# Performance work log

Measured on AMD Instinct MI355X. Metric: run time of the kernel, lower is better.

Reference implementation:

```python
import jax, jax.numpy as jnp
import numpy as np

EPS = float(np.finfo(np.float32).eps)
B, MZ, NF = 8192, 2000, 2048
W_INT, W_PROB, W_WS, W_MORGAN = 0.1, 0.3, 0.5, 0.1
POS_W = 5.0


def _bce_logits(x, y):
    # numerically-stable BCEWithLogits, elementwise
    return jnp.maximum(x, 0.0) - x * y + jnp.log1p(jnp.exp(-jnp.abs(x)))


def setup_inputs() -> dict:
    key = jax.random.key(0)
    k = jax.random.split(key, 6)
    return {
        "pred_intensities": jax.random.normal(k[0], (B, MZ), jnp.float32),
        "pred_probs_logits": jax.random.normal(k[1], (B, MZ), jnp.float32),
        "pred_morgan_logits": jax.random.normal(k[2], (B, NF), jnp.float32),
        "true_intensities": jax.random.uniform(k[3], (B, MZ), dtype=jnp.float32),
        "true_probs": jax.random.uniform(k[4], (B, MZ), dtype=jnp.float32),
        "true_morgan": jax.random.randint(k[5], (B, NF), 0, 2).astype(jnp.int32),
    }


def reference(pred_intensities, pred_probs_logits, pred_morgan_logits,
              true_intensities, true_probs, true_morgan):
    # --- prob loss: BCEWithLogits with positive-class upweighting ---
    bce = _bce_logits(pred_probs_logits, true_probs)
    w = jnp.where(true_probs > 0.5, POS_W, 1.0)
    prob_loss = jnp.mean(bce * w)

    # --- intensity loss: MSE masked to true peaks ---
    iw = (true_probs > 0.5).astype(jnp.float32)
    intensity_loss = jnp.sum(iw * (pred_intensities - true_intensities) ** 2) / (jnp.sum(iw) + EPS)

    # --- Wasserstein-1 loss (original detaches pred -> no grad; exact EMD on 1D
    #     grid with cost |i-j|/(MZ-1+EPS) == scaled L1 distance of CDFs) ---
    pred_prob = jax.nn.sigmoid(pred_probs_logits)
    pred_dist = jax.nn.relu(pred_intensities) * pred_prob
    pred_dist = pred_dist / (pred_dist.sum(axis=1, keepdims=True) + EPS)
    true_un = true_intensities * true_probs
    true_dist = true_un / (true_un.sum(axis=1, keepdims=True) + EPS)
    # per-sample renormalization as in the python loop
    p = pred_dist / (pred_dist.sum(axis=1, keepdims=True) + EPS)
    q = true_dist / (true_dist.sum(axis=1, keepdims=True) + EPS)
    scale = 1.0 / (float(MZ - 1) + EPS)  # cost matrix M = |i-j| / (max + EPS)
    cdf_diff = jnp.cumsum(p - q, axis=1)          # [B, MZ]
    w1 = jnp.sum(jnp.abs(cdf_diff[:, :-1]), axis=1) * scale  # exact 1D EMD
    psum = p.sum(axis=1)
    qsum = q.sum(axis=1)
    valid = (qsum > EPS).astype(jnp.float32)       # counted iff true mass > EPS
    per_sample = jnp.where(psum > EPS, w1, 1.0)    # pred degenerate -> penalty 1.0
    nvalid = jnp.sum(valid)
    ws_loss = jnp.where(nvalid > 0,
                        jnp.sum(per_sample * valid) / jnp.maximum(nvalid, 1.0),
                        0.0)
    ws_loss = jax.lax.stop_gradient(ws_loss)  # original converts to python float

    # --- morgan fingerprint loss: mean BCEWithLogits ---
    morgan_loss = jnp.mean(_bce_logits(pred_morgan_logits, true_morgan.astype(jnp.float32)))

    total = (W_PROB * prob_loss + W_INT * intensity_loss
             + W_WS * ws_loss + W_MORGAN * morgan_loss)
    total = jnp.where(jnp.isnan(total) | jnp.isinf(total), 100000.0, total)
    return total
```

## Files before the change

### kernel.cpp

```cpp
#include <hip/hip_runtime.h>
#include <cmath>

#define EPSF 1.1920928955078125e-07f

constexpr int BB = 8192;
constexpr int MZ = 2000;
constexpr int NF = 2048;
constexpr int MORGAN_BLOCKS = 2048;
constexpr int FUSED_BLOCKS = BB + MORGAN_BLOCKS;
constexpr float W_INT = 0.1f, W_PROB = 0.3f, W_WS = 0.5f, W_MORGAN = 0.1f;
constexpr float POS_W = 5.0f;

constexpr int PB_STRIDE = BB;
constexpr int PBM_OFF = 5 * BB;

__device__ inline float waveReduce(float v) {
#pragma unroll
  for (int off = 32; off > 0; off >>= 1) v += __shfl_down(v, off, 64);
  return v;
}

__device__ inline double waveReduceD(double v) {
#pragma unroll
  for (int off = 32; off > 0; off >>= 1) v += __shfl_down(v, off, 64);
  return v;
}

__device__ inline float bceFast(float x, float y) {
  const float em = __expf(-fabsf(x));
  return fmaxf(x, 0.f) - x * y + __logf(1.f + em);
}

__device__ inline void row_body(int bid, const float* __restrict__ pi,
                                const float* __restrict__ pl,
                                const float* __restrict__ ti,
                                const float* __restrict__ tp,
                                float* __restrict__ pb) {
  __shared__ float red[4][8];
  __shared__ float bc[2];
  __shared__ float wtot[4];

  const int tid = threadIdx.x;
  const int lane = tid & 63;
  const int wid = tid >> 6;
  const long base = (long)bid * MZ;
  const int i0 = tid * 8;

  float a[8], b[8];
  float s_bce = 0.f, s_sq = 0.f, s_iw = 0.f, la = 0.f, lb = 0.f;

  if (i0 + 8 <= MZ) {
    const float4* ppi = (const float4*)(pi + base + i0);
    const float4* ppl = (const float4*)(pl + base + i0);
    const float4* pti = (const float4*)(ti + base + i0);
    const float4* ptp = (const float4*)(tp + base + i0);
    float4 vpi0 = ppi[0], vpi1 = ppi[1];
    float4 vpl0 = ppl[0], vpl1 = ppl[1];
    float4 vti0 = pti[0], vti1 = pti[1];
    float4 vtp0 = ptp[0], vtp1 = ptp[1];
    float xpi[8] = {vpi0.x, vpi0.y, vpi0.z, vpi0.w, vpi1.x, vpi1.y, vpi1.z, vpi1.w};
    float xpl[8] = {vpl0.x, vpl0.y, vpl0.z, vpl0.w, vpl1.x, vpl1.y, vpl1.z, vpl1.w};
    float xti[8] = {vti0.x, vti0.y, vti0.z, vti0.w, vti1.x, vti1.y, vti1.z, vti1.w};
    float xtp[8] = {vtp0.x, vtp0.y, vtp0.z, vtp0.w, vtp1.x, vtp1.y, vtp1.z, vtp1.w};
#pragma unroll
    for (int j = 0; j < 8; ++j) {
      const float x = xpl[j];
      const float y = xtp[j];
      const float em = __expf(-fabsf(x));
      const float bce = fmaxf(x, 0.f) - x * y + __logf(1.f + em);
      const bool pos = (y > 0.5f);
      s_bce += bce * (pos ? POS_W : 1.f);
      const float d = xpi[j] - xti[j];
      if (pos) { s_sq = fmaf(d, d, s_sq); s_iw += 1.f; }
      const float inv = __builtin_amdgcn_rcpf(1.f + em);
      const float sig = (x >= 0.f) ? inv : em * inv;
      const float av = fmaxf(xpi[j], 0.f) * sig;
      const float bv = xti[j] * y;
      a[j] = av; b[j] = bv;
      la += av; lb += bv;
    }
  } else {
#pragma unroll
    for (int j = 0; j < 8; ++j) { a[j] = 0.f; b[j] = 0.f; }
  }

  float v0 = waveReduce(la);
  float v1 = waveReduce(lb);
  float v2 = waveReduce(s_bce);
  float v3 = waveReduce(s_sq);
  float v4 = waveReduce(s_iw);
  if (lane == 0) {
    red[wid][0] = v0; red[wid][1] = v1; red[wid][2] = v2;
    red[wid][3] = v3; red[wid][4] = v4;
  }
  __syncthreads();
  if (tid == 0) {
    const float s1  = red[0][0] + red[1][0] + red[2][0] + red[3][0];
    const float st1 = red[0][1] + red[1][1] + red[2][1] + red[3][1];
    bc[0] = s1; bc[1] = st1;
    pb[0 * PB_STRIDE + bid] = red[0][2] + red[1][2] + red[2][2] + red[3][2];
    pb[1 * PB_STRIDE + bid] = red[0][3] + red[1][3] + red[2][3] + red[3][3];
    pb[2 * PB_STRIDE + bid] = red[0][4] + red[1][4] + red[2][4] + red[3][4];
  }
  __syncthreads();
  const float s1 = bc[0], st1 = bc[1];

  const float s2 = s1 / (s1 + EPSF);
  const float scaleP = 1.f / ((s1 + EPSF) * (s2 + EPSF));
  const float st2 = st1 / (st1 + EPSF);
  const float scaleQ = 1.f / ((st1 + EPSF) * (st2 + EPSF));

  float run = 0.f;
#pragma unroll
  for (int j = 0; j < 8; ++j) {
    run += a[j] * scaleP - b[j] * scaleQ;
    a[j] = run;
  }

  float sc = run;
#pragma unroll
  for (int off = 1; off < 64; off <<= 1) {
    const float t = __shfl_up(sc, off, 64);
    if (lane >= off) sc += t;
  }
  if (lane == 63) wtot[wid] = sc;
  __syncthreads();
  float woff = 0.f;
#pragma unroll
  for (int w = 0; w < 4; ++w) woff += (w < wid) ? wtot[w] : 0.f;
  const float excl = sc - run + woff;

  float labs = 0.f;
#pragma unroll
  for (int j = 0; j < 8; ++j) {
    if (i0 + j < MZ - 1) labs += fabsf(excl + a[j]);
  }
  labs = waveReduce(labs);
  if (lane == 0) red[wid][0] = labs;
  __syncthreads();
  if (tid == 0) {
    const float t = red[0][0] + red[1][0] + red[2][0] + red[3][0];
    const float w1 = t * (1.f / (1999.0f + EPSF));
    const float psum = s2 / (s2 + EPSF);
    const float qsum = st2 / (st2 + EPSF);
    const float valid = (qsum > EPSF) ? 1.f : 0.f;
    const float per = (psum > EPSF) ? w1 : 1.f;
    pb[3 * PB_STRIDE + bid] = per * valid;
    pb[4 * PB_STRIDE + bid] = valid;
  }
}

__device__ inline void morgan_body(int mbid, const float* __restrict__ x,
                                   const int* __restrict__ y,
                                   float* __restrict__ pbm) {
  __shared__ float mred[4];
  const long n4 = (long)BB * NF / 4;
  const long stride = (long)MORGAN_BLOCKS * 256;
  float ls = 0.f;
  for (long i = (long)mbid * 256 + threadIdx.x; i < n4; i += stride) {
    const float4 xv = ((const float4*)x)[i];
    const int4 yv = ((const int4*)y)[i];
    ls += bceFast(xv.x, (float)yv.x);
    ls += bceFast(xv.y, (float)yv.y);
    ls += bceFast(xv.z, (float)yv.z);
    ls += bceFast(xv.w, (float)yv.w);
  }
  ls = waveReduce(ls);
  const int lane = threadIdx.x & 63, wid = threadIdx.x >> 6;
  if (lane == 0) mred[wid] = ls;
  __syncthreads();
  if (threadIdx.x == 0)
    pbm[mbid] = mred[0] + mred[1] + mred[2] + mred[3];
}

__global__ __launch_bounds__(256) void fused_kernel(
    const float* __restrict__ pi, const float* __restrict__ pl,
    const float* __restrict__ ti, const float* __restrict__ tp,
    const float* __restrict__ mx, const int* __restrict__ my,
    float* __restrict__ ws) {
  const int q = blockIdx.x / 5;
  const int r = blockIdx.x % 5;
  if (r < 4) {
    row_body(q * 4 + r, pi, pl, ti, tp, ws);
  } else {
    morgan_body(q, mx, my, ws + PBM_OFF);
  }
}

__global__ __launch_bounds__(1024) void reduce_finalize_kernel(
    const float* __restrict__ ws, float* __restrict__ out) {
  __shared__ double red[16][8];
  const int tid = threadIdx.x;
  const int lane = tid & 63, wid = tid >> 6;

  double acc[6] = {0, 0, 0, 0, 0, 0};
#pragma unroll
  for (int k = 0; k < 5; ++k) {
    const float4* v = (const float4*)(ws + k * PB_STRIDE);
    for (int i = tid; i < BB / 4; i += 1024) {
      const float4 f = v[i];
      acc[k] += (double)f.x + (double)f.y + (double)f.z + (double)f.w;
    }
  }
  {
    const float4* v = (const float4*)(ws + PBM_OFF);
    for (int i = tid; i < MORGAN_BLOCKS / 4; i += 1024) {
      const float4 f = v[i];
      acc[5] += (double)f.x + (double)f.y + (double)f.z + (double)f.w;
    }
  }

#pragma unroll
  for (int k = 0; k < 6; ++k) acc[k] = waveReduceD(acc[k]);
  if (lane == 0) {
#pragma unroll
    for (int k = 0; k < 6; ++k) red[wid][k] = acc[k];
  }
  __syncthreads();
  if (tid == 0) {
    double t[6];
#pragma unroll
    for (int k = 0; k < 6; ++k) {
      double s = 0.0;
      for (int w = 0; w < 16; ++w) s += red[w][k];
      t[k] = s;
    }
    const double prob = t[0] / ((double)BB * (double)MZ);
    const double inten = t[1] / (t[2] + (double)EPSF);
    const double nv = t[4];
    const double ws_loss = (nv > 0.0) ? (t[3] / fmax(nv, 1.0)) : 0.0;
    const double morgan = t[5] / ((double)BB * (double)NF);
    double tot = (double)W_PROB * prob + (double)W_INT * inten +
                 (double)W_WS * ws_loss + (double)W_MORGAN * morgan;
    float r = (float)tot;
    if (isnan(r) || isinf(r)) r = 100000.0f;
    out[0] = r;
  }
}

extern "C" void kernel_launch(void* const* d_in, const int* in_sizes, int n_in,
                              void* d_out, int out_size, void* d_ws, size_t ws_size,
                              hipStream_t stream) {
  const float* pred_int = (const float*)d_in[0];
  const float* pred_pl  = (const float*)d_in[1];
  const float* pred_mg  = (const float*)d_in[2];
  const float* true_int = (const float*)d_in[3];
  const float* true_pr  = (const float*)d_in[4];
  const int*   true_mg  = (const int*)d_in[5];
  float* ws = (float*)d_ws;

  fused_kernel<<<FUSED_BLOCKS, 256, 0, stream>>>(
      pred_int, pred_pl, true_int, true_pr, pred_mg, true_mg, ws);
  reduce_finalize_kernel<<<1, 1024, 0, stream>>>(ws, (float*)d_out);
}
```

Baseline: 348.6 us.

## Make row and morgan blocks persistent with software-prefetched row loads

Cuts the grid to 1024 row blocks of 8 rows each plus 512 morgan blocks, interleaved 2:1. Each row block loads the next row's data into registers while it computes the current row, so memory latency overlaps the barrier-heavy scan. The morgan loop now runs a fixed, unrolled trip count, and __syncthreads is replaced with a raw LDS wait plus s_barrier. In exchange the kernel uses more registers, has fewer blocks to hide latency, and adds one extra barrier per row.

```diff
diff --git a/kernel.cpp b/kernel.cpp
--- a/kernel.cpp
+++ b/kernel.cpp
@@ -6,13 +6,21 @@
 constexpr int BB = 8192;
 constexpr int MZ = 2000;
 constexpr int NF = 2048;
-constexpr int MORGAN_BLOCKS = 2048;
-constexpr int FUSED_BLOCKS = BB + MORGAN_BLOCKS;
+constexpr int ROW_BLOCKS = 1024;
+constexpr int ROWS_PER_BLOCK = 8;
+constexpr int MG_BLOCKS = 512;
+constexpr int MG_ITERS = (BB * NF / 4) / (MG_BLOCKS * 256);
 constexpr float W_INT = 0.1f, W_PROB = 0.3f, W_WS = 0.5f, W_MORGAN = 0.1f;
 constexpr float POS_W = 5.0f;
 
 constexpr int PB_STRIDE = BB;
 constexpr int PBM_OFF = 5 * BB;
+
+__device__ inline void ldsBarrier() {
+  asm volatile("s_waitcnt lgkmcnt(0)" ::: "memory");
+  __builtin_amdgcn_s_barrier();
+  asm volatile("" ::: "memory");
+}
 
 __device__ inline float waveReduce(float v) {
 #pragma unroll
@@ -31,11 +39,37 @@
   return fmaxf(x, 0.f) - x * y + __logf(1.f + em);
 }
 
-__device__ inline void row_body(int bid, const float* __restrict__ pi,
-                                const float* __restrict__ pl,
-                                const float* __restrict__ ti,
-                                const float* __restrict__ tp,
-                                float* __restrict__ pb) {
+struct RowData {
+  float4 pi0, pi1, pl0, pl1, ti0, ti1, tp0, tp1;
+};
+
+__device__ inline RowData zeroRow() {
+  RowData d;
+  const float4 z = make_float4(0.f, 0.f, 0.f, 0.f);
+  d.pi0 = z; d.pi1 = z; d.pl0 = z; d.pl1 = z;
+  d.ti0 = z; d.ti1 = z; d.tp0 = z; d.tp1 = z;
+  return d;
+}
+
+__device__ inline RowData loadRow(long base, int i0,
+                                  const float* __restrict__ pi,
+                                  const float* __restrict__ pl,
+                                  const float* __restrict__ ti,
+                                  const float* __restrict__ tp) {
+  RowData d;
+  const float4* ppi = (const float4*)(pi + base + i0);
+  const float4* ppl = (const float4*)(pl + base + i0);
+  const float4* pti = (const float4*)(ti + base + i0);
+  const float4* ptp = (const float4*)(tp + base + i0);
+  d.pi0 = ppi[0]; d.pi1 = ppi[1];
+  d.pl0 = ppl[0]; d.pl1 = ppl[1];
+  d.ti0 = pti[0]; d.ti1 = pti[1];
+  d.tp0 = ptp[0]; d.tp1 = ptp[1];
+  return d;
+}
+
+__device__ inline void computeRow(const RowData& dta, int bid, bool act,
+                                  float* __restrict__ pb) {
   __shared__ float red[4][8];
   __shared__ float bc[2];
   __shared__ float wtot[4];
@@ -43,25 +77,20 @@
   const int tid = threadIdx.x;
   const int lane = tid & 63;
   const int wid = tid >> 6;
-  const long base = (long)bid * MZ;
   const int i0 = tid * 8;
 
   float a[8], b[8];
   float s_bce = 0.f, s_sq = 0.f, s_iw = 0.f, la = 0.f, lb = 0.f;
 
-  if (i0 + 8 <= MZ) {
-    const float4* ppi = (const float4*)(pi + base + i0);
-    const float4* ppl = (const float4*)(pl + base + i0);
-    const float4* pti = (const float4*)(ti + base + i0);
-    const float4* ptp = (const float4*)(tp + base + i0);
-    float4 vpi0 = ppi[0], vpi1 = ppi[1];
-    float4 vpl0 = ppl[0], vpl1 = ppl[1];
-    float4 vti0 = pti[0], vti1 = pti[1];
-    float4 vtp0 = ptp[0], vtp1 = ptp[1];
-    float xpi[8] = {vpi0.x, vpi0.y, vpi0.z, vpi0.w, vpi1.x, vpi1.y, vpi1.z, vpi1.w};
-    float xpl[8] = {vpl0.x, vpl0.y, vpl0.z, vpl0.w, vpl1.x, vpl1.y, vpl1.z, vpl1.w};
-    float xti[8] = {vti0.x, vti0.y, vti0.z, vti0.w, vti1.x, vti1.y, vti1.z, vti1.w};
-    float xtp[8] = {vtp0.x, vtp0.y, vtp0.z, vtp0.w, vtp1.x, vtp1.y, vtp1.z, vtp1.w};
+  if (act) {
+    float xpi[8] = {dta.pi0.x, dta.pi0.y, dta.pi0.z, dta.pi0.w,
+                    dta.pi1.x, dta.pi1.y, dta.pi1.z, dta.pi1.w};
+    float xpl[8] = {dta.pl0.x, dta.pl0.y, dta.pl0.z, dta.pl0.w,
+                    dta.pl1.x, dta.pl1.y, dta.pl1.z, dta.pl1.w};
+    float xti[8] = {dta.ti0.x, dta.ti0.y, dta.ti0.z, dta.ti0.w,
+                    dta.ti1.x, dta.ti1.y, dta.ti1.z, dta.ti1.w};
+    float xtp[8] = {dta.tp0.x, dta.tp0.y, dta.tp0.z, dta.tp0.w,
+                    dta.tp1.x, dta.tp1.y, dta.tp1.z, dta.tp1.w};
 #pragma unroll
     for (int j = 0; j < 8; ++j) {
       const float x = xpl[j];
@@ -93,7 +122,7 @@
     red[wid][0] = v0; red[wid][1] = v1; red[wid][2] = v2;
     red[wid][3] = v3; red[wid][4] = v4;
   }
-  __syncthreads();
+  ldsBarrier();
   if (tid == 0) {
     const float s1  = red[0][0] + red[1][0] + red[2][0] + red[3][0];
     const float st1 = red[0][1] + red[1][1] + red[2][1] + red[3][1];
@@ -102,7 +131,7 @@
     pb[1 * PB_STRIDE + bid] = red[0][3] + red[1][3] + red[2][3] + red[3][3];
     pb[2 * PB_STRIDE + bid] = red[0][4] + red[1][4] + red[2][4] + red[3][4];
   }
-  __syncthreads();
+  ldsBarrier();
   const float s1 = bc[0], st1 = bc[1];
 
   const float s2 = s1 / (s1 + EPSF);
@@ -124,7 +153,7 @@
     if (lane >= off) sc += t;
   }
   if (lane == 63) wtot[wid] = sc;
-  __syncthreads();
+  ldsBarrier();
   float woff = 0.f;
 #pragma unroll
   for (int w = 0; w < 4; ++w) woff += (w < wid) ? wtot[w] : 0.f;
@@ -137,7 +166,7 @@
   }
   labs = waveReduce(labs);
   if (lane == 0) red[wid][0] = labs;
-  __syncthreads();
+  ldsBarrier();
   if (tid == 0) {
     const float t = red[0][0] + red[1][0] + red[2][0] + red[3][0];
     const float w1 = t * (1.f / (1999.0f + EPSF));
@@ -148,16 +177,40 @@
     pb[3 * PB_STRIDE + bid] = per * valid;
     pb[4 * PB_STRIDE + bid] = valid;
   }
-}
-
-__device__ inline void morgan_body(int mbid, const float* __restrict__ x,
-                                   const int* __restrict__ y,
-                                   float* __restrict__ pbm) {
+  ldsBarrier();
+}
+
+__device__ inline void rowPersistent(int blk,
+                                     const float* __restrict__ pi,
+                                     const float* __restrict__ pl,
+                                     const float* __restrict__ ti,
+                                     const float* __restrict__ tp,
+                                     float* __restrict__ pb) {
+  const int i0 = threadIdx.x * 8;
+  const bool act = (i0 + 8 <= MZ);
+  const int row0 = blk * ROWS_PER_BLOCK;
+
+  RowData A = act ? loadRow((long)row0 * MZ, i0, pi, pl, ti, tp) : zeroRow();
+#pragma unroll
+  for (int i = 0; i < ROWS_PER_BLOCK - 1; ++i) {
+    RowData B = act ? loadRow((long)(row0 + i + 1) * MZ, i0, pi, pl, ti, tp)
+                    : zeroRow();
+    computeRow(A, row0 + i, act, pb);
+    A = B;
+  }
+  computeRow(A, row0 + ROWS_PER_BLOCK - 1, act, pb);
+}
+
+__device__ inline void morganPersistent(int mbid,
+                                        const float* __restrict__ x,
+                                        const int* __restrict__ y,
+                                        float* __restrict__ pbm) {
   __shared__ float mred[4];
-  const long n4 = (long)BB * NF / 4;
-  const long stride = (long)MORGAN_BLOCKS * 256;
+  const long stride = (long)MG_BLOCKS * 256;
   float ls = 0.f;
-  for (long i = (long)mbid * 256 + threadIdx.x; i < n4; i += stride) {
+  long i = (long)mbid * 256 + threadIdx.x;
+#pragma unroll 4
+  for (int it = 0; it < MG_ITERS; ++it, i += stride) {
     const float4 xv = ((const float4*)x)[i];
     const int4 yv = ((const int4*)y)[i];
     ls += bceFast(xv.x, (float)yv.x);
@@ -168,7 +221,7 @@
   ls = waveReduce(ls);
   const int lane = threadIdx.x & 63, wid = threadIdx.x >> 6;
   if (lane == 0) mred[wid] = ls;
-  __syncthreads();
+  ldsBarrier();
   if (threadIdx.x == 0)
     pbm[mbid] = mred[0] + mred[1] + mred[2] + mred[3];
 }
@@ -178,12 +231,12 @@
     const float* __restrict__ ti, const float* __restrict__ tp,
     const float* __restrict__ mx, const int* __restrict__ my,
     float* __restrict__ ws) {
-  const int q = blockIdx.x / 5;
-  const int r = blockIdx.x % 5;
-  if (r < 4) {
-    row_body(q * 4 + r, pi, pl, ti, tp, ws);
+  const int q = blockIdx.x / 3;
+  const int r = blockIdx.x % 3;
+  if (r < 2) {
+    rowPersistent(q * 2 + r, pi, pl, ti, tp, ws);
   } else {
-    morgan_body(q, mx, my, ws + PBM_OFF);
+    morganPersistent(q, mx, my, ws + PBM_OFF);
   }
 }
 
@@ -204,7 +257,7 @@
   }
   {
     const float4* v = (const float4*)(ws + PBM_OFF);
-    for (int i = tid; i < MORGAN_BLOCKS / 4; i += 1024) {
+    for (int i = tid; i < MG_BLOCKS / 4; i += 1024) {
       const float4 f = v[i];
       acc[5] += (double)f.x + (double)f.y + (double)f.z + (double)f.w;
     }
@@ -249,7 +302,7 @@
   const int*   true_mg  = (const int*)d_in[5];
   float* ws = (float*)d_ws;
 
-  fused_kernel<<<FUSED_BLOCKS, 256, 0, stream>>>(
+  fused_kernel<<<ROW_BLOCKS + MG_BLOCKS, 256, 0, stream>>>(
       pred_int, pred_pl, true_int, true_pr, pred_mg, true_mg, ws);
   reduce_finalize_kernel<<<1, 1024, 0, stream>>>(ws, (float*)d_out);
 }
```

New measurement: 372.6 us. +6.9%, slower.

## Process one row per wavefront to remove block-level syncs and LDS reductions

Applied to the files above, without the earlier changes.

Each spectrum row is now handled by a single 64-lane wavefront with 32 elements per lane, so all reductions and the prefix scan use only wave shuffles, with no __syncthreads or shared memory. Row blocks drop from 8192 to 2048, each holding four rows. The morgan part uses 1024 blocks with a fixed unrolled trip count and writes per-wave partials. In exchange, each lane needs many more registers for the 32-element a/b arrays, which can lower occupancy, and each lane's loads are less coalesced (32 contiguous floats per lane).

```diff
diff --git a/kernel.cpp b/kernel.cpp
--- a/kernel.cpp
+++ b/kernel.cpp
@@ -6,17 +6,20 @@
 constexpr int BB = 8192;
 constexpr int MZ = 2000;
 constexpr int NF = 2048;
-constexpr int MORGAN_BLOCKS = 2048;
-constexpr int FUSED_BLOCKS = BB + MORGAN_BLOCKS;
+constexpr int ROW_BLOCKS = 2048;
+constexpr int MG_BLOCKS = 1024;
+constexpr int MG_ITERS = (BB * NF / 4) / (MG_BLOCKS * 256);
+constexpr int TOTAL_BLOCKS = ROW_BLOCKS + MG_BLOCKS;
 constexpr float W_INT = 0.1f, W_PROB = 0.3f, W_WS = 0.5f, W_MORGAN = 0.1f;
 constexpr float POS_W = 5.0f;
 
 constexpr int PB_STRIDE = BB;
 constexpr int PBM_OFF = 5 * BB;
-
-__device__ inline float waveReduce(float v) {
-#pragma unroll
-  for (int off = 32; off > 0; off >>= 1) v += __shfl_down(v, off, 64);
+constexpr int PBM_N = MG_BLOCKS * 4;
+
+__device__ inline float waveAllSum(float v) {
+#pragma unroll
+  for (int off = 1; off < 64; off <<= 1) v += __shfl_xor(v, off, 64);
   return v;
 }
 
@@ -31,80 +34,64 @@
   return fmaxf(x, 0.f) - x * y + __logf(1.f + em);
 }
 
-__device__ inline void row_body(int bid, const float* __restrict__ pi,
-                                const float* __restrict__ pl,
-                                const float* __restrict__ ti,
-                                const float* __restrict__ tp,
-                                float* __restrict__ pb) {
-  __shared__ float red[4][8];
-  __shared__ float bc[2];
-  __shared__ float wtot[4];
-
-  const int tid = threadIdx.x;
-  const int lane = tid & 63;
-  const int wid = tid >> 6;
-  const long base = (long)bid * MZ;
-  const int i0 = tid * 8;
-
-  float a[8], b[8];
+__device__ void rowWave(int row,
+                        const float* __restrict__ pi, const float* __restrict__ pl,
+                        const float* __restrict__ ti, const float* __restrict__ tp,
+                        float* __restrict__ pb) {
+  const int lane = threadIdx.x & 63;
+  const int cbase = lane * 32;
+  const long base = (long)row * MZ + cbase;
+
+  float a[32], b[32];
   float s_bce = 0.f, s_sq = 0.f, s_iw = 0.f, la = 0.f, lb = 0.f;
 
-  if (i0 + 8 <= MZ) {
-    const float4* ppi = (const float4*)(pi + base + i0);
-    const float4* ppl = (const float4*)(pl + base + i0);
-    const float4* pti = (const float4*)(ti + base + i0);
-    const float4* ptp = (const float4*)(tp + base + i0);
-    float4 vpi0 = ppi[0], vpi1 = ppi[1];
-    float4 vpl0 = ppl[0], vpl1 = ppl[1];
-    float4 vti0 = pti[0], vti1 = pti[1];
-    float4 vtp0 = ptp[0], vtp1 = ptp[1];
-    float xpi[8] = {vpi0.x, vpi0.y, vpi0.z, vpi0.w, vpi1.x, vpi1.y, vpi1.z, vpi1.w};
-    float xpl[8] = {vpl0.x, vpl0.y, vpl0.z, vpl0.w, vpl1.x, vpl1.y, vpl1.z, vpl1.w};
-    float xti[8] = {vti0.x, vti0.y, vti0.z, vti0.w, vti1.x, vti1.y, vti1.z, vti1.w};
-    float xtp[8] = {vtp0.x, vtp0.y, vtp0.z, vtp0.w, vtp1.x, vtp1.y, vtp1.z, vtp1.w};
-#pragma unroll
-    for (int j = 0; j < 8; ++j) {
-      const float x = xpl[j];
-      const float y = xtp[j];
-      const float em = __expf(-fabsf(x));
-      const float bce = fmaxf(x, 0.f) - x * y + __logf(1.f + em);
-      const bool pos = (y > 0.5f);
-      s_bce += bce * (pos ? POS_W : 1.f);
-      const float d = xpi[j] - xti[j];
-      if (pos) { s_sq = fmaf(d, d, s_sq); s_iw += 1.f; }
-      const float inv = __builtin_amdgcn_rcpf(1.f + em);
-      const float sig = (x >= 0.f) ? inv : em * inv;
-      const float av = fmaxf(xpi[j], 0.f) * sig;
-      const float bv = xti[j] * y;
-      a[j] = av; b[j] = bv;
-      la += av; lb += bv;
-    }
-  } else {
-#pragma unroll
-    for (int j = 0; j < 8; ++j) { a[j] = 0.f; b[j] = 0.f; }
-  }
-
-  float v0 = waveReduce(la);
-  float v1 = waveReduce(lb);
-  float v2 = waveReduce(s_bce);
-  float v3 = waveReduce(s_sq);
-  float v4 = waveReduce(s_iw);
+#pragma unroll
+  for (int g = 0; g < 8; ++g) {
+    const int e0 = cbase + g * 4;
+    if (e0 + 4 <= MZ) {
+      const float4 vpi = *(const float4*)(pi + base + g * 4);
+      const float4 vpl = *(const float4*)(pl + base + g * 4);
+      const float4 vti = *(const float4*)(ti + base + g * 4);
+      const float4 vtp = *(const float4*)(tp + base + g * 4);
+      const float xpi[4] = {vpi.x, vpi.y, vpi.z, vpi.w};
+      const float xpl[4] = {vpl.x, vpl.y, vpl.z, vpl.w};
+      const float xti[4] = {vti.x, vti.y, vti.z, vti.w};
+      const float xtp[4] = {vtp.x, vtp.y, vtp.z, vtp.w};
+#pragma unroll
+      for (int k = 0; k < 4; ++k) {
+        const float x = xpl[k];
+        const float y = xtp[k];
+        const float em = __expf(-fabsf(x));
+        const float bce = fmaxf(x, 0.f) - x * y + __logf(1.f + em);
+        const bool pos = (y > 0.5f);
+        s_bce += bce * (pos ? POS_W : 1.f);
+        const float d = xpi[k] - xti[k];
+        if (pos) { s_sq = fmaf(d, d, s_sq); s_iw += 1.f; }
+        const float inv = __builtin_amdgcn_rcpf(1.f + em);
+        const float sig = (x >= 0.f) ? inv : em * inv;
+        const float av = fmaxf(xpi[k], 0.f) * sig;
+        const float bv = xti[k] * y;
+        a[g * 4 + k] = av; b[g * 4 + k] = bv;
+        la += av; lb += bv;
+      }
+    } else {
+#pragma unroll
+      for (int k = 0; k < 4; ++k) { a[g * 4 + k] = 0.f; b[g * 4 + k] = 0.f; }
+    }
+  }
+
+  la = waveAllSum(la);
+  lb = waveAllSum(lb);
+  s_bce = waveAllSum(s_bce);
+  s_sq = waveAllSum(s_sq);
+  s_iw = waveAllSum(s_iw);
   if (lane == 0) {
-    red[wid][0] = v0; red[wid][1] = v1; red[wid][2] = v2;
-    red[wid][3] = v3; red[wid][4] = v4;
-  }
-  __syncthreads();
-  if (tid == 0) {
-    const float s1  = red[0][0] + red[1][0] + red[2][0] + red[3][0];
-    const float st1 = red[0][1] + red[1][1] + red[2][1] + red[3][1];
-    bc[0] = s1; bc[1] = st1;
-    pb[0 * PB_STRIDE + bid] = red[0][2] + red[1][2] + red[2][2] + red[3][2];
-    pb[1 * PB_STRIDE + bid] = red[0][3] + red[1][3] + red[2][3] + red[3][3];
-    pb[2 * PB_STRIDE + bid] = red[0][4] + red[1][4] + red[2][4] + red[3][4];
-  }
-  __syncthreads();
-  const float s1 = bc[0], st1 = bc[1];
-
+    pb[0 * PB_STRIDE + row] = s_bce;
+    pb[1 * PB_STRIDE + row] = s_sq;
+    pb[2 * PB_STRIDE + row] = s_iw;
+  }
+
+  const float s1 = la, st1 = lb;
   const float s2 = s1 / (s1 + EPSF);
   const float scaleP = 1.f / ((s1 + EPSF) * (s2 + EPSF));
   const float st2 = st1 / (st1 + EPSF);
@@ -112,7 +99,7 @@
 
   float run = 0.f;
 #pragma unroll
-  for (int j = 0; j < 8; ++j) {
+  for (int j = 0; j < 32; ++j) {
     run += a[j] * scaleP - b[j] * scaleQ;
     a[j] = run;
   }
@@ -123,41 +110,35 @@
     const float t = __shfl_up(sc, off, 64);
     if (lane >= off) sc += t;
   }
-  if (lane == 63) wtot[wid] = sc;
-  __syncthreads();
-  float woff = 0.f;
-#pragma unroll
-  for (int w = 0; w < 4; ++w) woff += (w < wid) ? wtot[w] : 0.f;
-  const float excl = sc - run + woff;
+  const float excl = sc - run;
 
   float labs = 0.f;
 #pragma unroll
-  for (int j = 0; j < 8; ++j) {
-    if (i0 + j < MZ - 1) labs += fabsf(excl + a[j]);
-  }
-  labs = waveReduce(labs);
-  if (lane == 0) red[wid][0] = labs;
-  __syncthreads();
-  if (tid == 0) {
-    const float t = red[0][0] + red[1][0] + red[2][0] + red[3][0];
-    const float w1 = t * (1.f / (1999.0f + EPSF));
+  for (int j = 0; j < 32; ++j) {
+    if (cbase + j < MZ - 1) labs += fabsf(excl + a[j]);
+  }
+  labs = waveAllSum(labs);
+
+  if (lane == 0) {
+    const float w1 = labs * (1.f / (1999.0f + EPSF));
     const float psum = s2 / (s2 + EPSF);
     const float qsum = st2 / (st2 + EPSF);
     const float valid = (qsum > EPSF) ? 1.f : 0.f;
     const float per = (psum > EPSF) ? w1 : 1.f;
-    pb[3 * PB_STRIDE + bid] = per * valid;
-    pb[4 * PB_STRIDE + bid] = valid;
-  }
-}
-
-__device__ inline void morgan_body(int mbid, const float* __restrict__ x,
-                                   const int* __restrict__ y,
-                                   float* __restrict__ pbm) {
-  __shared__ float mred[4];
-  const long n4 = (long)BB * NF / 4;
-  const long stride = (long)MORGAN_BLOCKS * 256;
+    pb[3 * PB_STRIDE + row] = per * valid;
+    pb[4 * PB_STRIDE + row] = valid;
+  }
+}
+
+__device__ void morganBlock(int mb, const float* __restrict__ x,
+                            const int* __restrict__ y, float* __restrict__ pbm) {
+  const int wid = threadIdx.x >> 6;
+  const int lane = threadIdx.x & 63;
   float ls = 0.f;
-  for (long i = (long)mbid * 256 + threadIdx.x; i < n4; i += stride) {
+  long i = (long)mb * 256 + threadIdx.x;
+  const long stride = (long)MG_BLOCKS * 256;
+#pragma unroll 4
+  for (int it = 0; it < MG_ITERS; ++it, i += stride) {
     const float4 xv = ((const float4*)x)[i];
     const int4 yv = ((const int4*)y)[i];
     ls += bceFast(xv.x, (float)yv.x);
@@ -165,12 +146,8 @@
     ls += bceFast(xv.z, (float)yv.z);
     ls += bceFast(xv.w, (float)yv.w);
   }
-  ls = waveReduce(ls);
-  const int lane = threadIdx.x & 63, wid = threadIdx.x >> 6;
-  if (lane == 0) mred[wid] = ls;
-  __syncthreads();
-  if (threadIdx.x == 0)
-    pbm[mbid] = mred[0] + mred[1] + mred[2] + mred[3];
+  ls = waveAllSum(ls);
+  if (lane == 0) pbm[mb * 4 + wid] = ls;
 }
 
 __global__ __launch_bounds__(256) void fused_kernel(
@@ -178,12 +155,14 @@
     const float* __restrict__ ti, const float* __restrict__ tp,
     const float* __restrict__ mx, const int* __restrict__ my,
     float* __restrict__ ws) {
-  const int q = blockIdx.x / 5;
-  const int r = blockIdx.x % 5;
-  if (r < 4) {
-    row_body(q * 4 + r, pi, pl, ti, tp, ws);
+  const int q = blockIdx.x / 3;
+  const int r = blockIdx.x % 3;
+  if (r < 2) {
+    const int rb = q * 2 + r;
+    const int row = rb * 4 + (threadIdx.x >> 6);
+    rowWave(row, pi, pl, ti, tp, ws);
   } else {
-    morgan_body(q, mx, my, ws + PBM_OFF);
+    morganBlock(q, mx, my, ws + PBM_OFF);
   }
 }
 
@@ -204,7 +183,7 @@
   }
   {
     const float4* v = (const float4*)(ws + PBM_OFF);
-    for (int i = tid; i < MORGAN_BLOCKS / 4; i += 1024) {
+    for (int i = tid; i < PBM_N / 4; i += 1024) {
       const float4 f = v[i];
       acc[5] += (double)f.x + (double)f.y + (double)f.z + (double)f.w;
     }
@@ -249,7 +228,7 @@
   const int*   true_mg  = (const int*)d_in[5];
   float* ws = (float*)d_ws;
 
-  fused_kernel<<<FUSED_BLOCKS, 256, 0, stream>>>(
+  fused_kernel<<<TOTAL_BLOCKS, 256, 0, stream>>>(
       pred_int, pred_pl, true_int, true_pr, pred_mg, true_mg, ws);
   reduce_finalize_kernel<<<1, 1024, 0, stream>>>(ws, (float*)d_out);
 }
```

Result: slower. 504.5 us (+44.7%).
